# Kernel optimization log

Measured on AMD Instinct MI355X. Metric: run time of the kernel, lower is better.

The kernel has to match this reference:

```python
import jax, jax.numpy as jnp
import numpy as np

ALPHA = 200.0      # cfg.TRAIN.VOTING_ALPHA
RHO = 100.0        # ADMM penalty
SIGMA = 1e-3       # ADMM regularization
ITERS = 150        # fixed ADMM iterations


def _admm_qp(Q, q, C, l, u):
    n = Q.shape[0]
    K = Q + SIGMA * jnp.eye(n, dtype=Q.dtype) + RHO * (C.T @ C)
    cf = jax.scipy.linalg.cho_factor(K)
    x0 = jnp.zeros((n,), Q.dtype)
    z0 = jnp.clip(jnp.zeros((C.shape[0],), Q.dtype), l, u)
    y0 = jnp.zeros((C.shape[0],), Q.dtype)

    def step(carry, _):
        x, z, y = carry
        rhs = SIGMA * x - q + C.T @ (RHO * z - y)
        x = jax.scipy.linalg.cho_solve(cf, rhs)
        Cx = C @ x
        z = jnp.clip(Cx + y / RHO, l, u)
        y = y + RHO * (Cx - z)
        return (x, z, y), None

    (x, _, _), _ = jax.lax.scan(step, (x0, z0, y0), None, length=ITERS)
    return x


def _l2n(x, axis):
    return x / jnp.maximum(jnp.linalg.norm(x, axis=axis, keepdims=True), 1e-12)


def _forward(feat_tra, feat_det, iou_mat, W, b):
    n1, d = feat_tra.shape
    n2 = feat_det.shape[0]
    # cross-graph feature update
    Mp0 = feat_tra @ feat_det.T + iou_mat                      # (n1,n2)
    m1 = Mp0 @ feat_det                                        # (n1,d)
    m2 = Mp0.T @ feat_tra                                      # (n2,d)
    lam1 = jax.lax.stop_gradient(jnp.linalg.norm(feat_tra, axis=1, keepdims=True)
                                 / jnp.linalg.norm(m1, axis=1, keepdims=True))
    lam2 = jax.lax.stop_gradient(jnp.linalg.norm(feat_det, axis=1, keepdims=True)
                                 / jnp.linalg.norm(m2, axis=1, keepdims=True))
    e1 = jax.nn.relu((feat_tra + lam1 * m1) @ W.T + b)
    e2 = jax.nn.relu((feat_det + lam2 * m2) @ W.T + b)
    e1 = _l2n(e1, 1)
    e2 = _l2n(e2, 1)
    Mp = e1 @ e2.T                                             # (n1,n2) unary affinity
    P = Mp.T                                                   # (n2,n1)
    # Quadratic affinity: the torch code builds src_tgt[i,j,k,l] = <cat(e1_i,e1_j), cat(e2_k,e2_l)>
    # = Mp[i,k] + Mp[j,l], then gathers M[(a,c),(b,d)] = src_tgt[c,d,a,b]/2 masked by (a!=b)&(c!=d).
    ms = 1.0 - jnp.eye(n1, dtype=Mp.dtype)
    mt = 1.0 - jnp.eye(n2, dtype=Mp.dtype)
    M4 = 0.5 * (P[:, :, None, None] + P[None, None, :, :]) \
         * (mt[:, None, :, None] * ms[None, :, None, :])       # (n2,n1,n2,n1)
    n = n1 * n2
    Q = float((n1 - 1) * (n2 - 1)) * jnp.eye(n, dtype=Mp.dtype) - M4.reshape(n, n)
    q = -P.reshape(-1)                                         # -Mpp
    # equality constraints (square case): column sums and row sums == 1
    A = jnp.concatenate([jnp.kron(jnp.ones((1, n1)), jnp.eye(n2)),
                         jnp.kron(jnp.eye(n1), jnp.ones((1, n2)))], axis=0).astype(Mp.dtype)
    C = jnp.concatenate([jnp.eye(n, dtype=Mp.dtype), A], axis=0)
    l = jnp.concatenate([jnp.zeros((n,), Mp.dtype), jnp.ones((n1 + n2,), Mp.dtype)])
    u = jnp.concatenate([jnp.full((n,), 1e6, Mp.dtype), jnp.ones((n1 + n2,), Mp.dtype)])
    x = _admm_qp(Q, q, C, l, u)
    s = x.reshape(n2, n1).T                                    # (n1,n2)
    s = jnp.clip(s, 0.0, 1.0)                                  # relu(s) - relu(s-1)
    s = jax.nn.softmax(ALPHA * s, axis=-1)                     # Voting layer
    return s[None]                                             # (1,n1,n2)


def setup_inputs() -> dict:
    key = jax.random.key(0)
    k1, k2, k3, k4 = jax.random.split(key, 4)
    n1 = n2 = 64
    d = 512
    feat_tra = jax.random.normal(k1, (n1, d), jnp.float32)
    feat_det = jax.random.normal(k2, (n2, d), jnp.float32)
    iou_mat = jax.random.uniform(k3, (n1, n2), jnp.float32)
    W = jnp.eye(d, dtype=jnp.float32) + 0.01 * jax.random.normal(k4, (d, d), jnp.float32)
    b = jnp.zeros((d,), jnp.float32)
    return {"feat_tra": feat_tra, "feat_det": feat_det, "iou_mat": iou_mat, "W": W, "b": b}


def reference(feat_tra, feat_det, iou_mat, W, b):
    return _forward(feat_tra, feat_det, iou_mat, W, b)
```

## Files before the change

kernel.cpp:

```cpp
#include <hip/hip_runtime.h>
#include <math.h>

#define DD 512
#define NS 258
#define NSP 264
#define NWG 64
#define BLK 1024
#define RHO_ 100.0
#define SIG_ 1e-3
#define NITER 150
#define DELTA0 (3969.0 + SIG_ + RHO_)

typedef float v2f __attribute__((ext_vector_type(2)));

#define OFF_E1     512u
#define OFF_SUMS   512u
#define OFF_INV    4608u
#define OFF_E2     262656u
#define OFF_P      524800u
#define OFF_W      557568u
#define OFF_P32    590336u
#define OFF_W32    606720u
#define OFF_KSA    623104u
#define OFF_KSB    1168000u
#define OFF_N32    1712896u

__device__ __forceinline__ int perm258(int i){
  return (i < 128) ? i : (i == 128) ? 256 : (i == 129) ? 257 : (i - 2);
}

template<int CTRL>
__device__ __forceinline__ float dppadd(float v){
  int t = __builtin_amdgcn_mov_dpp(__float_as_int(v), CTRL, 0xF, 0xF, 1);
  return v + __int_as_float(t);
}
template<int CTRL>
__device__ __forceinline__ float dppmax(float v){
  int t = __builtin_amdgcn_mov_dpp(__float_as_int(v), CTRL, 0xF, 0xF, 1);
  return fmaxf(v, __int_as_float(t));
}
__device__ __forceinline__ float sum16(float v){
  v = dppadd<0xB1>(v);
  v = dppadd<0x4E>(v);
  v = dppadd<0x124>(v);
  v = dppadd<0x128>(v);
  return v;
}
__device__ __forceinline__ float wsum64f(float v){
  v = sum16(v);
  v += __shfl_xor(v, 16, 64);
  v += __shfl_xor(v, 32, 64);
  return v;
}
__device__ __forceinline__ float wmax64f(float v){
  v = dppmax<0xB1>(v); v = dppmax<0x4E>(v); v = dppmax<0x124>(v); v = dppmax<0x128>(v);
  v = fmaxf(v, __shfl_xor(v, 16, 64));
  v = fmaxf(v, __shfl_xor(v, 32, 64));
  return v;
}

__device__ __forceinline__ double gsum16d(double v){
  v += __shfl_xor(v, 1, 64);
  v += __shfl_xor(v, 2, 64);
  v += __shfl_xor(v, 4, 64);
  v += __shfl_xor(v, 8, 64);
  return v;
}
__device__ __forceinline__ double wsum64d(double v){
  v = gsum16d(v);
  v += __shfl_xor(v, 16, 64);
  v += __shfl_xor(v, 32, 64);
  return v;
}

__device__ __forceinline__ void decode_idx(int t, int& cls, int& pr, int& ix){
  if (t < 64)       { cls = 1; pr = 1; ix = t; }
  else if (t < 128) { cls = 2; pr = 1; ix = t - 64; }
  else if (t == 128){ cls = 0; pr = 1; ix = 0; }
  else if (t == 129){ cls = 0; pr = 0; ix = 0; }
  else if (t < 194) { cls = 1; pr = 0; ix = t - 130; }
  else              { cls = 2; pr = 0; ix = t - 194; }
}

__device__ __forceinline__ double ksval(int r, int c, const double* __restrict__ p,
                                        const double* __restrict__ w, const double* sumsL){
  int cr, prr, ir, cc, prc, ic;
  decode_idx(r, cr, prr, ir);
  decode_idx(c, cc, prc, ic);
  int m = prr + prc;
  double tval;
  if (cr == 0 && cc == 0)      tval = sumsL[m];
  else if (cr == 0 && cc == 1) tval = sumsL[8 + m*64 + ic];
  else if (cr == 1 && cc == 0) tval = sumsL[8 + m*64 + ir];
  else if (cr == 0 && cc == 2) tval = sumsL[200 + m*64 + ic];
  else if (cr == 2 && cc == 0) tval = sumsL[200 + m*64 + ir];
  else if (cr == 1 && cc == 1) tval = (ir == ic) ? sumsL[8 + m*64 + ir] : 0.0;
  else if (cr == 2 && cc == 2) tval = (ir == ic) ? sumsL[200 + m*64 + ir] : 0.0;
  else if (cr == 1 && cc == 2){
    double wv = w[ic*64 + ir], pv = p[ic*64 + ir];
    tval = (m == 0) ? wv : (m == 1) ? wv*pv : wv*pv*pv;
  } else {
    double wv = w[ir*64 + ic], pv = p[ir*64 + ic];
    tval = (m == 0) ? wv : (m == 1) ? wv*pv : wv*pv*pv;
  }
  double mv2 = 0.0;
  if (cr == 0 && cc == 0 && prr != prc) mv2 = -2.0;
  if (cr != 0 && cr == cc && ir == ic){
    if (prr != prc) mv2 = 2.0;
    else if (prr == 1) mv2 = -4.0 * RHO_;
  }
  return tval + mv2;
}

__global__ __launch_bounds__(BLK) void kp_feat(const float* __restrict__ ft,
                                               const float* __restrict__ fd,
                                               const float* __restrict__ iou,
                                               const float* __restrict__ Wm,
                                               const float* __restrict__ bb,
                                               char* ws){
  double* e1 = (double*)(ws + OFF_E1);
  double* e2 = (double*)(ws + OFF_E2);
  __shared__ double SH[1192];
  const int tid  = threadIdx.x;
  const int wg   = blockIdx.x;
  const int lane = tid & 63;
  const int wv   = tid >> 6;
  float* ftR = (float*)SH;
  float* fdR = ftR + 512;
  float* u1R = fdR + 512;
  float* u2R = u1R + 512;
  double* m0r = SH + 1024;
  double* m0c = m0r + 64;
  double* wp  = m0c + 64;
  double* sca = wp + 32;
  const int i = wg;
  if (tid < 512){ ftR[tid] = ft[i*DD + tid]; fdR[tid] = fd[i*DD + tid]; }
  {
    double nf = 0.0, nd = 0.0;
    if (tid < 512){
      float a = ftR[tid], b = fdR[tid];
      nf = (double)a*a; nd = (double)b*b;
    }
    nf = wsum64d(nf); nd = wsum64d(nd);
    if (lane == 0){ wp[wv] = nf; wp[16 + wv] = nd; }
    __syncthreads();
    if (tid == 0){
      double s0 = 0, s1 = 0;
      for (int q = 0; q < 16; ++q){ s0 += wp[q]; s1 += wp[16+q]; }
      sca[0] = s0; sca[1] = s1;
    }
  }
  {
    int j = tid >> 4, sub = tid & 15;
    double ar = 0.0, ac = 0.0;
    for (int t2 = 0; t2 < 32; ++t2){
      int k = t2*16 + sub;
      ar += (double)ftR[k] * (double)fd[(size_t)j*DD + k];
      ac += (double)fdR[k] * (double)ft[(size_t)j*DD + k];
    }
    ar = gsum16d(ar); ac = gsum16d(ac);
    if (sub == 0){
      m0r[j] = ar + (double)iou[i*64 + j];
      m0c[j] = ac + (double)iou[j*64 + i];
    }
  }
  __syncthreads();
  {
    int c = tid & 511, half = tid >> 9;
    const double* m0 = half ? m0c : m0r;
    const float*  FB = half ? ft  : fd;
    double a0 = 0, b0 = 0, c0 = 0, d0 = 0;
    for (int a2 = 0; a2 < 64; a2 += 4){
      a0 += m0[a2]   * (double)FB[(size_t)(a2  )*DD + c];
      b0 += m0[a2+1] * (double)FB[(size_t)(a2+1)*DD + c];
      c0 += m0[a2+2] * (double)FB[(size_t)(a2+2)*DD + c];
      d0 += m0[a2+3] * (double)FB[(size_t)(a2+3)*DD + c];
    }
    double mv = (a0 + b0) + (c0 + d0);
    double nn = wsum64d(mv*mv);
    if (lane == 0) wp[wv] = nn;
    __syncthreads();
    if (tid < 2){
      double s = 0;
      for (int q = tid*8; q < tid*8 + 8; ++q) s += wp[q];
      sca[2 + tid] = sqrt(sca[tid] / s);
    }
    __syncthreads();
    double l = sca[2 + half];
    float* uR = half ? u2R : u1R;
    const float* fR = half ? fdR : ftR;
    uR[c] = (float)((double)fR[c] + l*mv);
  }
  __syncthreads();
  {
    int c = tid & 511, half = tid >> 9;
    const float* uR  = half ? u2R : u1R;
    const float* wrp = Wm + (size_t)c*DD;
    double a0 = (double)bb[c], b0 = 0, c0 = 0, d0 = 0;
    for (int k = 0; k < DD; k += 4){
      float4 wq = *(const float4*)(wrp + k);
      float4 uq = *(const float4*)(uR + k);
      a0 += (double)uq.x*wq.x; b0 += (double)uq.y*wq.y;
      c0 += (double)uq.z*wq.z; d0 += (double)uq.w*wq.w;
    }
    double v = fmax((a0 + b0) + (c0 + d0), 0.0);
    double nn = wsum64d(v*v);
    if (lane == 0) wp[wv] = nn;
    __syncthreads();
    if (tid < 2){
      double s = 0;
      for (int q = tid*8; q < tid*8 + 8; ++q) s += wp[q];
      sca[4 + tid] = 1.0 / fmax(sqrt(s), 1e-12);
    }
    __syncthreads();
    double* e = half ? e2 : e1;
    e[(size_t)i*DD + c] = v * sca[4 + half];
  }
}

__global__ __launch_bounds__(BLK) void kp_pw(char* ws){
  const double* e1 = (const double*)(ws + OFF_E1);
  const double* e2 = (const double*)(ws + OFF_E2);
  double* p   = (double*)(ws + OFF_P);
  double* w   = (double*)(ws + OFF_W);
  float*  p32 = (float*) (ws + OFF_P32);
  float*  w32 = (float*) (ws + OFF_W32);
  __shared__ double e2R[512];
  const int tid = threadIdx.x;
  const int a = blockIdx.x;
  if (tid < 512) e2R[tid] = e2[(size_t)a*DD + tid];
  __syncthreads();
  int b = tid >> 4, sub = tid & 15;
  double a0 = 0.0, a1 = 0.0;
  for (int t2 = 0; t2 < 32; t2 += 2){
    a0 += e1[(size_t)b*DD + t2*16 + sub]     * e2R[t2*16 + sub];
    a1 += e1[(size_t)b*DD + (t2+1)*16 + sub] * e2R[(t2+1)*16 + sub];
  }
  double acc = gsum16d(a0 + a1);
  if (sub == 0){
    double pv = acc;
    double wv2 = 1.0 / (DELTA0 - pv);
    int jj = a*64 + b;
    p[jj] = pv; w[jj] = wv2; p32[jj] = (float)pv; w32[jj] = (float)wv2;
  }
}

__global__ __launch_bounds__(BLK) void kp_sums(char* ws){
  const double* p = (const double*)(ws + OFF_P);
  const double* w = (const double*)(ws + OFF_W);
  double* sumsG = (double*)(ws + OFF_SUMS);
  __shared__ double sumsL[456];
  const int tid = threadIdx.x;
  int a = tid >> 4, sub = tid & 15;
  {
    double r0 = 0, r1 = 0, r2 = 0;
    for (int b = sub*4; b < sub*4 + 4; ++b){
      double wv = w[a*64 + b], pv = p[a*64 + b];
      r0 += wv; r1 += wv*pv; r2 += wv*pv*pv;
    }
    r0 = gsum16d(r0); r1 = gsum16d(r1); r2 = gsum16d(r2);
    if (sub == 0){ sumsL[200 + a] = r0; sumsL[264 + a] = r1; sumsL[328 + a] = r2; }
  }
  {
    int b2 = tid >> 4;
    double c0 = 0, c1 = 0, c2 = 0;
    for (int a2 = sub*4; a2 < sub*4 + 4; ++a2){
      double wv = w[a2*64 + b2], pv = p[a2*64 + b2];
      c0 += wv; c1 += wv*pv; c2 += wv*pv*pv;
    }
    c0 = gsum16d(c0); c1 = gsum16d(c1); c2 = gsum16d(c2);
    if (sub == 0){ sumsL[8 + b2] = c0; sumsL[72 + b2] = c1; sumsL[136 + b2] = c2; }
  }
  __syncthreads();
  if (tid == 0){
    double t0 = 0, t1 = 0, t2 = 0;
    for (int a3 = 0; a3 < 64; ++a3){
      t0 += sumsL[200 + a3]; t1 += sumsL[264 + a3]; t2 += sumsL[328 + a3];
    }
    sumsL[0] = t0; sumsL[1] = t1; sumsL[2] = t2;
    sumsL[3] = 0; sumsL[4] = 0; sumsL[5] = 0; sumsL[6] = 0; sumsL[7] = 0;
  }
  if (tid >= 64 && tid < 128){
    int k = tid - 64;
    sumsL[392 + k] = 1.0 / (sumsL[136 + k] - 4.0*RHO_);
  }
  __syncthreads();
  for (int idx = tid; idx < 456; idx += BLK) sumsG[idx] = sumsL[idx];
}

template<int NC>
__device__ void p3_body(const double* __restrict__ p, const double* __restrict__ w,
                        const double* sumsL, const double* invd, double* temp,
                        double* __restrict__ KsB, int wg, int tid){
  if (tid < NC*64){
    int cidx = tid >> 6, k = tid & 63;
    int c = wg + 256*cidx;
    double tv;
    if (c < 64) tv = (k == c) ? invd[k] : 0.0;
    else        tv = ksval(k, c, p, w, sumsL) * invd[k];
    temp[cidx*68 + k] = tv;
  }
  __syncthreads();
  for (int idx = tid; idx < NS*NC; idx += BLK){
    int r = idx / NC, cidx = idx % NC;
    int c = wg + 256*cidx;
    double outv;
    if (r < 64){
      outv = temp[cidx*68 + r];
    } else {
      double first = (c < 64) ? 0.0 : ksval(r, c, p, w, sumsL);
      double acc = 0.0;
      const double* tp = temp + cidx*68;
      if (r < 128){
        const double* wr_ = w + (r-64)*64;
        const double* pr_ = p + (r-64)*64;
#pragma unroll 4
        for (int k = 0; k < 64; ++k){
          double pv = pr_[k];
          acc += wr_[k]*pv*pv*tp[k];
        }
      } else if (r == 128){
#pragma unroll 4
        for (int k = 0; k < 64; ++k) acc += sumsL[136 + k]*tp[k];
      } else if (r == 129){
#pragma unroll 4
        for (int k = 0; k < 64; ++k) acc += sumsL[72 + k]*tp[k];
      } else if (r < 194){
        int ir = r - 130;
        acc = (sumsL[72 + ir] + 2.0) * tp[ir];
      } else {
        int ir = r - 194;
        const double* wr_ = w + ir*64;
        const double* pr_ = p + ir*64;
#pragma unroll 4
        for (int k = 0; k < 64; ++k) acc += wr_[k]*pr_[k]*tp[k];
      }
      outv = first - acc;
    }
    KsB[(size_t)r*NSP + c] = outv;
  }
}

__global__ __launch_bounds__(BLK) void kp_p3(char* ws){
  const double* p = (const double*)(ws + OFF_P);
  const double* w = (const double*)(ws + OFF_W);
  const double* sumsG = (const double*)(ws + OFF_SUMS);
  double* KsB = (double*)(ws + OFF_KSB);
  __shared__ double sumsL[456];
  __shared__ double temp[136];
  const int tid = threadIdx.x, wg = blockIdx.x;
  for (int idx = tid; idx < 456; idx += BLK) sumsL[idx] = sumsG[idx];
  __syncthreads();
  if (wg < 2) p3_body<2>(p, w, sumsL, sumsL + 392, temp, KsB, wg, tid);
  else        p3_body<1>(p, w, sumsL, sumsL + 392, temp, KsB, wg, tid);
}

template<int MM>
__global__ __launch_bounds__(BLK) void kp_inv(const double* __restrict__ src, int p0,
                                              double* __restrict__ invG){
  __shared__ double Mbuf[2*4422];
  const int tid = threadIdx.x;
  double* cur = Mbuf;
  double* nxt = Mbuf + 4422;
  for (int idx = tid; idx < MM*MM; idx += BLK)
    cur[(idx/MM)*67 + (idx%MM)] = src[(size_t)(p0 + idx/MM)*NSP + p0 + idx%MM];
  __syncthreads();
  for (int k = 0; k < MM; ++k){
    double pk = 1.0 / cur[k*67 + k];
    for (int idx = tid; idx < MM*MM; idx += BLK){
      int i = idx/MM, j = idx%MM;
      double mkj = cur[k*67 + j];
      double nv;
      if (i == k){
        nv = (j == k) ? pk : mkj*pk;
      } else {
        double mik = cur[i*67 + k];
        nv = (j == k) ? (-mik*pk) : (cur[i*67 + j] - mik*(mkj*pk));
      }
      nxt[i*67 + j] = nv;
    }
    __syncthreads();
    double* t = cur; cur = nxt; nxt = t;
  }
  for (int idx = tid; idx < MM*MM; idx += BLK)
    invG[(idx/MM)*67 + idx%MM] = cur[(idx/MM)*67 + idx%MM];
}

template<int NC, int MM>
__device__ void apply_body(const double* __restrict__ src, double* __restrict__ dstD,
                           float* __restrict__ dstF, int p0, int wg, int tid,
                           const double* M, double* temp){
  for (int idx = tid; idx < NC*MM; idx += BLK){
    int cidx = idx / MM, k = idx % MM;
    int c = wg + 256*cidx;
    double tv;
    if (c >= p0 && c < p0 + MM){
      tv = M[k*67 + (c - p0)];
    } else {
      double a0 = 0.0, a1 = 0.0;
#pragma unroll 4
      for (int l = 0; l < MM; l += 2){
        a0 += M[k*67 + l]     * src[(size_t)(p0+l)*NSP + c];
        a1 += M[k*67 + l + 1] * src[(size_t)(p0+l+1)*NSP + c];
      }
      tv = a0 + a1;
    }
    temp[cidx*68 + k] = tv;
  }
  __syncthreads();
  for (int idx = tid; idx < NS*NC; idx += BLK){
    int r = idx / NC, cidx = idx % NC;
    int c = wg + 256*cidx;
    double val;
    if (r >= p0 && r < p0 + MM){
      val = temp[cidx*68 + (r - p0)];
    } else {
      double a0 = (c >= p0 && c < p0 + MM) ? 0.0 : src[(size_t)r*NSP + c];
      double a1 = 0.0;
#pragma unroll 4
      for (int k = 0; k < MM; k += 2){
        a0 -= src[(size_t)r*NSP + p0 + k]     * temp[cidx*68 + k];
        a1 += src[(size_t)r*NSP + p0 + k + 1] * temp[cidx*68 + k + 1];
      }
      val = a0 - a1;
    }
    if (dstD) dstD[(size_t)r*NSP + c] = val;
    else      dstF[perm258(r)*NSP + perm258(c)] = (float)val;
  }
}

template<int MM>
__global__ __launch_bounds__(BLK) void kp_apply(const double* __restrict__ src,
                                                double* __restrict__ dstD,
                                                float* __restrict__ dstF, int p0,
                                                const double* __restrict__ invG){
  __shared__ double M[4422];
  __shared__ double temp[136];
  const int tid = threadIdx.x, wg = blockIdx.x;
  for (int idx = tid; idx < MM*67; idx += BLK) M[idx] = invG[idx];
  __syncthreads();
  if (wg < 2) apply_body<2, MM>(src, dstD, dstF, p0, wg, tid, M, temp);
  else        apply_body<1, MM>(src, dstD, dstF, p0, wg, tid, M, temp);
}

__global__ __launch_bounds__(BLK) __attribute__((amdgpu_waves_per_eu(4, 4)))
void k_admm(const float* __restrict__ N32,
            const float* __restrict__ p32,
            const float* __restrict__ w32,
            float* __restrict__ out){
  __shared__ float2 tb[64][66];
  __shared__ float2 csTP[64][18];
  __shared__ float  csXl[64][18];
  __shared__ __align__(16) float s1f[264];
  __shared__ float s1g2[2];
  __shared__ float s2g[2];
  __shared__ __align__(16) float s2p[4][264];
  __shared__ float2 pairB[64];
  __shared__ float2 pairR[64];

  const int tid  = threadIdx.x;
  const int lane = tid & 63;
  const int wvid = tid >> 6;
  const int g    = tid >> 8;
  const int c    = tid & 255;

  float4 nc4[16];
#pragma unroll
  for (int k2 = 0; k2 < 16; ++k2){
    nc4[k2].x = N32[(64*g + 4*k2 + 0)*NSP + c];
    nc4[k2].y = N32[(64*g + 4*k2 + 1)*NSP + c];
    nc4[k2].z = N32[(64*g + 4*k2 + 2)*NSP + c];
    nc4[k2].w = N32[(64*g + 4*k2 + 3)*NSP + c];
  }
  const float ncg0 = N32[256*NSP + c];
  const float ncg1 = N32[257*NSP + c];

  float nr0 = 0.f, nr1 = 0.f, nr2 = 0.f, nr3 = 0.f, nrt0 = 0.f, nrt1 = 0.f;
  if (wvid == 4 || wvid == 5){
    int r = 252 + wvid;
    nr0 = N32[r*NSP + lane];       nr1 = N32[r*NSP + lane + 64];
    nr2 = N32[r*NSP + lane + 128]; nr3 = N32[r*NSP + lane + 192];
    nrt0 = N32[r*NSP + 256];       nrt1 = N32[r*NSP + 257];
  }

  float pr[4], wr[4], xr[4], vr[4], tq[4];
  double y2a[4], y2b = 0.0;
#pragma unroll
  for (int q = 0; q < 4; ++q){
    int j = (wvid*4 + q)*64 + lane;
    pr[q] = p32[j]; wr[q] = w32[j];
    xr[q] = 0.f; vr[q] = 0.f; tq[q] = 0.f; y2a[q] = 0.0;
  }
  __syncthreads();

  const int rid = tid >> 4, g16 = tid & 15;

  for (int it = 0; it < NITER; ++it){
    if (it){
      float ybs = 0.f;
#pragma unroll
      for (int s = 0; s < 8; ++s){
        float2 v2 = *(const float2*)&csXl[lane][2*s];
        ybs += v2.x + v2.y;
      }
      y2b += RHO_ * ((double)ybs - 1.0);
    }
    float base = (float)(2.0*RHO_ - y2b);
    float clt = 0.f, clp = 0.f;
#pragma unroll
    for (int q = 0; q < 4; ++q){
      float ya = (float)y2a[q];
      float rhs = 1e-3f*xr[q] + pr[q] + 100.f*fabsf(vr[q]) + base - ya;
      float t = wr[q]*rhs;
      float pt = pr[q]*t;
      tq[q] = t;
      tb[wvid*4 + q][lane] = make_float2(t, pt);
      clt += t; clp += pt;
    }
    csTP[lane][(wvid + lane) & 15] = make_float2(clt, clp);
    __syncthreads();

    {
      const float4 r0 = *(const float4*)&tb[rid][4*g16];
      const float4 r1 = *(const float4*)&tb[rid][4*g16 + 2];
      float st = (r0.x + r0.z) + (r1.x + r1.z);
      float sp = (r0.y + r0.w) + (r1.y + r1.w);
      st = sum16(st); sp = sum16(sp);
      if (g16 == (rid & 15)){ s1f[192 + rid] = st; s1f[64 + rid] = sp; }
      if (wvid == 0){
        float ct = 0.f, cp = 0.f;
#pragma unroll
        for (int s = 0; s < 8; ++s){
          float4 v4 = *(const float4*)&csTP[lane][2*s];
          ct += v4.x + v4.z; cp += v4.y + v4.w;
        }
        s1f[128 + lane] = ct; s1f[lane] = cp;
        float tt = wsum64f(ct);
        float tp = wsum64f(cp);
        if (lane == 0){ s1g2[1] = tt; s1g2[0] = tp; }
      }
    }
    __syncthreads();

    {
      float sv = s1f[64*g + lane];
      float a0 = 0.f, a1 = 0.f, a2 = 0.f, a3 = 0.f;
#pragma unroll
      for (int k2 = 0; k2 < 16; ++k2){
        float4 nq = nc4[k2];
        a0 += nq.x * __uint_as_float(__builtin_amdgcn_readlane(__float_as_uint(sv), 4*k2 + 0));
        a1 += nq.y * __uint_as_float(__builtin_amdgcn_readlane(__float_as_uint(sv), 4*k2 + 1));
        a2 += nq.z * __uint_as_float(__builtin_amdgcn_readlane(__float_as_uint(sv), 4*k2 + 2));
        a3 += nq.w * __uint_as_float(__builtin_amdgcn_readlane(__float_as_uint(sv), 4*k2 + 3));
      }
      float acc = (a0 + a1) + (a2 + a3);
      if (g == 0) acc += ncg0*s1g2[0] + ncg1*s1g2[1];
      s2p[g][c] = acc;
      if (wvid == 4 || wvid == 5){
        float a32 = nr0*s1f[lane] + nr1*s1f[lane+64]
                  + nr2*s1f[lane+128] + nr3*s1f[lane+192];
        a32 = wsum64f(a32);
        if (lane == 0) s2g[wvid - 4] = a32 + nrt0*s1g2[0] + nrt1*s1g2[1];
      }
    }
    __syncthreads();

    if (tid < 64){
      int b = tid;
      float sbE  = (s2p[0][128+b] + s2p[1][128+b]) + (s2p[2][128+b] + s2p[3][128+b]);
      float sbPE = (s2p[0][b] + s2p[1][b]) + (s2p[2][b] + s2p[3][b]);
      pairB[b] = make_float2(sbE, sbPE);
    } else if (tid < 128){
      int a = tid - 64;
      float sF  = (s2p[0][192+a] + s2p[1][192+a]) + (s2p[2][192+a] + s2p[3][192+a]);
      float sPF = (s2p[0][64+a] + s2p[1][64+a]) + (s2p[2][64+a] + s2p[3][64+a]);
      pairR[a] = make_float2(s2g[1] + sF, s2g[0] + sPF);
    }
    __syncthreads();

    {
      float2 pb = pairB[lane];
      float clx = 0.f;
#pragma unroll
      for (int q = 0; q < 4; ++q){
        int arow = wvid*4 + q;
        float2 prw = pairR[arow];
        float corr = prw.x + pb.x + pr[q]*(prw.y + pb.y);
        float xn = tq[q] - wr[q]*corr;
        vr[q] = xn + fminf(vr[q], 0.f);
        xr[q] = xn;
        float rsx = wsum64f(xn);
        y2a[q] += RHO_*((double)rsx - 1.0);
        clx += xn;
        if (it == NITER-1) ((float*)tb)[lane*68 + arow] = xn;
      }
      csXl[lane][(wvid + lane) & 15] = clx;
    }
    __syncthreads();
  }

  const float* xb = (const float*)tb;
#pragma unroll
  for (int q = 0; q < 4; ++q){
    int i = wvid*4 + q;
    float val = xb[i*68 + lane];
    val = fminf(fmaxf(val, 0.f), 1.f);
    float mx = wmax64f(val);
    float e = expf(200.f*(val - mx));
    float sm = wsum64f(e);
    out[i*64 + lane] = e / sm;
  }
}

extern "C" void kernel_launch(void* const* d_in, const int* in_sizes, int n_in,
                              void* d_out, int out_size, void* d_ws, size_t ws_size,
                              hipStream_t stream){
  (void)in_sizes; (void)n_in; (void)out_size; (void)ws_size;
  const float* ft  = (const float*)d_in[0];
  const float* fd  = (const float*)d_in[1];
  const float* iou = (const float*)d_in[2];
  const float* Wm  = (const float*)d_in[3];
  const float* bb  = (const float*)d_in[4];
  char* ws = (char*)d_ws;

  double* KsA  = (double*)(ws + OFF_KSA);
  double* KsB  = (double*)(ws + OFF_KSB);
  double* invG = (double*)(ws + OFF_INV);
  float*  N32  = (float*) (ws + OFF_N32);

  hipLaunchKernelGGL(kp_feat, dim3(NWG), dim3(BLK), 0, stream, ft, fd, iou, Wm, bb, ws);
  hipLaunchKernelGGL(kp_pw,   dim3(NWG), dim3(BLK), 0, stream, ws);
  hipLaunchKernelGGL(kp_sums, dim3(1),   dim3(BLK), 0, stream, ws);
  hipLaunchKernelGGL(kp_p3,   dim3(256), dim3(BLK), 0, stream, ws);

  hipLaunchKernelGGL(kp_inv<66>,   dim3(1),   dim3(BLK), 0, stream, KsB, 64, invG);
  hipLaunchKernelGGL(kp_apply<66>, dim3(256), dim3(BLK), 0, stream, KsB, KsA, (float*)nullptr, 64, invG);
  hipLaunchKernelGGL(kp_inv<64>,   dim3(1),   dim3(BLK), 0, stream, KsA, 130, invG);
  hipLaunchKernelGGL(kp_apply<64>, dim3(256), dim3(BLK), 0, stream, KsA, KsB, (float*)nullptr, 130, invG);
  hipLaunchKernelGGL(kp_inv<64>,   dim3(1),   dim3(BLK), 0, stream, KsB, 194, invG);
  hipLaunchKernelGGL(kp_apply<64>, dim3(256), dim3(BLK), 0, stream, KsB, (double*)nullptr, N32, 194, invG);

  const float* p32 = (const float*)(ws + OFF_P32);
  const float* w32 = (const float*)(ws + OFF_W32);
  hipLaunchKernelGGL(k_admm, dim3(1), dim3(BLK), 0, stream, N32, p32, w32, (float*)d_out);
}
```

Before: 807.7 us.

## Use one block per column with split-k reductions; atomics and DPP sums in ADMM loop

The p3 and apply kernels now launch one block per column (258 blocks) rather than 256 blocks with two columns on the first two. Each row's dot product is split over 4 lanes (8 for the apply temp vector) and combined with shuffles, so per-thread serial loops get shorter. In the ADMM loop, per-group partial sums go to a single shared array through shared-memory atomicAdd, removing one reduction pass and one barrier per iteration. Wave sums now use row-broadcast DPP plus readlane. The atomics change the float summation order and add LDS contention.

```diff
diff --git a/kernel.cpp b/kernel.cpp
--- a/kernel.cpp
+++ b/kernel.cpp
@@ -51,6 +51,12 @@
   v += __shfl_xor(v, 16, 64);
   v += __shfl_xor(v, 32, 64);
   return v;
+}
+__device__ __forceinline__ float wsum64u(float v){
+  v = sum16(v);
+  v = dppadd<0x142>(v);
+  v = dppadd<0x143>(v);
+  return __uint_as_float(__builtin_amdgcn_readlane(__float_as_uint(v), 63));
 }
 __device__ __forceinline__ float wmax64f(float v){
   v = dppmax<0xB1>(v); v = dppmax<0x4E>(v); v = dppmax<0x124>(v); v = dppmax<0x128>(v);
@@ -288,71 +294,56 @@
   for (int idx = tid; idx < 456; idx += BLK) sumsG[idx] = sumsL[idx];
 }
 
-template<int NC>
-__device__ void p3_body(const double* __restrict__ p, const double* __restrict__ w,
-                        const double* sumsL, const double* invd, double* temp,
-                        double* __restrict__ KsB, int wg, int tid){
-  if (tid < NC*64){
-    int cidx = tid >> 6, k = tid & 63;
-    int c = wg + 256*cidx;
-    double tv;
-    if (c < 64) tv = (k == c) ? invd[k] : 0.0;
-    else        tv = ksval(k, c, p, w, sumsL) * invd[k];
-    temp[cidx*68 + k] = tv;
-  }
-  __syncthreads();
-  for (int idx = tid; idx < NS*NC; idx += BLK){
-    int r = idx / NC, cidx = idx % NC;
-    int c = wg + 256*cidx;
-    double outv;
-    if (r < 64){
-      outv = temp[cidx*68 + r];
-    } else {
-      double first = (c < 64) ? 0.0 : ksval(r, c, p, w, sumsL);
-      double acc = 0.0;
-      const double* tp = temp + cidx*68;
-      if (r < 128){
-        const double* wr_ = w + (r-64)*64;
-        const double* pr_ = p + (r-64)*64;
-#pragma unroll 4
-        for (int k = 0; k < 64; ++k){
-          double pv = pr_[k];
-          acc += wr_[k]*pv*pv*tp[k];
-        }
-      } else if (r == 128){
-#pragma unroll 4
-        for (int k = 0; k < 64; ++k) acc += sumsL[136 + k]*tp[k];
-      } else if (r == 129){
-#pragma unroll 4
-        for (int k = 0; k < 64; ++k) acc += sumsL[72 + k]*tp[k];
-      } else if (r < 194){
-        int ir = r - 130;
-        acc = (sumsL[72 + ir] + 2.0) * tp[ir];
-      } else {
-        int ir = r - 194;
-        const double* wr_ = w + ir*64;
-        const double* pr_ = p + ir*64;
-#pragma unroll 4
-        for (int k = 0; k < 64; ++k) acc += wr_[k]*pr_[k]*tp[k];
-      }
-      outv = first - acc;
-    }
-    KsB[(size_t)r*NSP + c] = outv;
-  }
-}
-
 __global__ __launch_bounds__(BLK) void kp_p3(char* ws){
   const double* p = (const double*)(ws + OFF_P);
   const double* w = (const double*)(ws + OFF_W);
   const double* sumsG = (const double*)(ws + OFF_SUMS);
   double* KsB = (double*)(ws + OFF_KSB);
   __shared__ double sumsL[456];
-  __shared__ double temp[136];
-  const int tid = threadIdx.x, wg = blockIdx.x;
+  __shared__ double temp[68];
+  const int tid = threadIdx.x;
+  const int c = blockIdx.x;
   for (int idx = tid; idx < 456; idx += BLK) sumsL[idx] = sumsG[idx];
   __syncthreads();
-  if (wg < 2) p3_body<2>(p, w, sumsL, sumsL + 392, temp, KsB, wg, tid);
-  else        p3_body<1>(p, w, sumsL, sumsL + 392, temp, KsB, wg, tid);
+  const double* invd = sumsL + 392;
+  if (tid < 64){
+    int k = tid;
+    temp[k] = (c < 64) ? ((k == c) ? invd[k] : 0.0) : ksval(k, c, p, w, sumsL) * invd[k];
+  }
+  __syncthreads();
+  const double* tp = temp;
+  const int s = tid & 3;
+  auto dorow = [&](int rr){
+    if (rr < 64){
+      if (s == 0) KsB[(size_t)rr*NSP + c] = tp[rr];
+      return;
+    }
+    double acc = 0.0;
+    if (rr < 128){
+      const double* wr_ = w + (rr-64)*64;
+      const double* pr_ = p + (rr-64)*64;
+      for (int k = s; k < 64; k += 4){ double pv = pr_[k]; acc += wr_[k]*pv*pv*tp[k]; }
+    } else if (rr == 128){
+      for (int k = s; k < 64; k += 4) acc += sumsL[136 + k]*tp[k];
+    } else if (rr == 129){
+      for (int k = s; k < 64; k += 4) acc += sumsL[72 + k]*tp[k];
+    } else if (rr < 194){
+      if (s == 0){ int ir = rr - 130; acc = (sumsL[72 + ir] + 2.0)*tp[ir]; }
+    } else {
+      int ir = rr - 194;
+      const double* wr_ = w + ir*64;
+      const double* pr_ = p + ir*64;
+      for (int k = s; k < 64; k += 4) acc += wr_[k]*pr_[k]*tp[k];
+    }
+    acc += __shfl_xor(acc, 1, 64);
+    acc += __shfl_xor(acc, 2, 64);
+    if (s == 0){
+      double first = (c < 64) ? 0.0 : ksval(rr, c, p, w, sumsL);
+      KsB[(size_t)rr*NSP + c] = first - acc;
+    }
+  };
+  { int r = tid >> 2; if (r < 256) dorow(r); }
+  if (tid < 8) dorow(256 + (tid >> 2));
 }
 
 template<int MM>
@@ -386,61 +377,57 @@
     invG[(idx/MM)*67 + idx%MM] = cur[(idx/MM)*67 + idx%MM];
 }
 
-template<int NC, int MM>
-__device__ void apply_body(const double* __restrict__ src, double* __restrict__ dstD,
-                           float* __restrict__ dstF, int p0, int wg, int tid,
-                           const double* M, double* temp){
-  for (int idx = tid; idx < NC*MM; idx += BLK){
-    int cidx = idx / MM, k = idx % MM;
-    int c = wg + 256*cidx;
-    double tv;
-    if (c >= p0 && c < p0 + MM){
-      tv = M[k*67 + (c - p0)];
-    } else {
-      double a0 = 0.0, a1 = 0.0;
-#pragma unroll 4
-      for (int l = 0; l < MM; l += 2){
-        a0 += M[k*67 + l]     * src[(size_t)(p0+l)*NSP + c];
-        a1 += M[k*67 + l + 1] * src[(size_t)(p0+l+1)*NSP + c];
-      }
-      tv = a0 + a1;
-    }
-    temp[cidx*68 + k] = tv;
-  }
-  __syncthreads();
-  for (int idx = tid; idx < NS*NC; idx += BLK){
-    int r = idx / NC, cidx = idx % NC;
-    int c = wg + 256*cidx;
-    double val;
-    if (r >= p0 && r < p0 + MM){
-      val = temp[cidx*68 + (r - p0)];
-    } else {
-      double a0 = (c >= p0 && c < p0 + MM) ? 0.0 : src[(size_t)r*NSP + c];
-      double a1 = 0.0;
-#pragma unroll 4
-      for (int k = 0; k < MM; k += 2){
-        a0 -= src[(size_t)r*NSP + p0 + k]     * temp[cidx*68 + k];
-        a1 += src[(size_t)r*NSP + p0 + k + 1] * temp[cidx*68 + k + 1];
-      }
-      val = a0 - a1;
-    }
-    if (dstD) dstD[(size_t)r*NSP + c] = val;
-    else      dstF[perm258(r)*NSP + perm258(c)] = (float)val;
-  }
-}
-
 template<int MM>
 __global__ __launch_bounds__(BLK) void kp_apply(const double* __restrict__ src,
                                                 double* __restrict__ dstD,
                                                 float* __restrict__ dstF, int p0,
                                                 const double* __restrict__ invG){
   __shared__ double M[4422];
-  __shared__ double temp[136];
-  const int tid = threadIdx.x, wg = blockIdx.x;
+  __shared__ double temp[68];
+  __shared__ double srcMid[66];
+  const int tid = threadIdx.x;
+  const int c = blockIdx.x;
   for (int idx = tid; idx < MM*67; idx += BLK) M[idx] = invG[idx];
-  __syncthreads();
-  if (wg < 2) apply_body<2, MM>(src, dstD, dstF, p0, wg, tid, M, temp);
-  else        apply_body<1, MM>(src, dstD, dstF, p0, wg, tid, M, temp);
+  if (tid < MM) srcMid[tid] = src[(size_t)(p0 + tid)*NSP + c];
+  __syncthreads();
+  const bool cpiv = (c >= p0 && c < p0 + MM);
+  if (cpiv){
+    if (tid < MM) temp[tid] = M[tid*67 + (c - p0)];
+  } else {
+    int k = tid >> 3, s8 = tid & 7;
+    if (k < MM){
+      double a = 0.0;
+      for (int l = s8; l < MM; l += 8) a += M[k*67 + l]*srcMid[l];
+      a += __shfl_xor(a, 1, 64);
+      a += __shfl_xor(a, 2, 64);
+      a += __shfl_xor(a, 4, 64);
+      if (s8 == 0) temp[k] = a;
+    }
+  }
+  __syncthreads();
+  const int s = tid & 3;
+  auto dorow = [&](int rr){
+    if (rr >= p0 && rr < p0 + MM){
+      if (s == 0){
+        double val = temp[rr - p0];
+        if (dstD) dstD[(size_t)rr*NSP + c] = val;
+        else      dstF[perm258(rr)*NSP + perm258(c)] = (float)val;
+      }
+      return;
+    }
+    double acc = 0.0;
+    for (int k = s; k < MM; k += 4) acc += src[(size_t)rr*NSP + p0 + k]*temp[k];
+    acc += __shfl_xor(acc, 1, 64);
+    acc += __shfl_xor(acc, 2, 64);
+    if (s == 0){
+      double f = cpiv ? 0.0 : src[(size_t)rr*NSP + c];
+      double val = f - acc;
+      if (dstD) dstD[(size_t)rr*NSP + c] = val;
+      else      dstF[perm258(rr)*NSP + perm258(c)] = (float)val;
+    }
+  };
+  { int r = tid >> 2; if (r < 256) dorow(r); }
+  if (tid < 8) dorow(256 + (tid >> 2));
 }
 
 __global__ __launch_bounds__(BLK) __attribute__((amdgpu_waves_per_eu(4, 4)))
@@ -454,9 +441,7 @@
   __shared__ __align__(16) float s1f[264];
   __shared__ float s1g2[2];
   __shared__ float s2g[2];
-  __shared__ __align__(16) float s2p[4][264];
-  __shared__ float2 pairB[64];
-  __shared__ float2 pairR[64];
+  __shared__ float s2s[264];
 
   const int tid  = threadIdx.x;
   const int lane = tid & 63;
@@ -518,6 +503,7 @@
       clt += t; clp += pt;
     }
     csTP[lane][(wvid + lane) & 15] = make_float2(clt, clp);
+    if (tid < 264) s2s[tid] = 0.f;
     __syncthreads();
 
     {
@@ -535,8 +521,8 @@
           ct += v4.x + v4.z; cp += v4.y + v4.w;
         }
         s1f[128 + lane] = ct; s1f[lane] = cp;
-        float tt = wsum64f(ct);
-        float tp = wsum64f(cp);
+        float tt = wsum64u(ct);
+        float tp = wsum64u(cp);
         if (lane == 0){ s1g2[1] = tt; s1g2[0] = tp; }
       }
     }
@@ -555,41 +541,31 @@
       }
       float acc = (a0 + a1) + (a2 + a3);
       if (g == 0) acc += ncg0*s1g2[0] + ncg1*s1g2[1];
-      s2p[g][c] = acc;
+      atomicAdd(&s2s[c], acc);
       if (wvid == 4 || wvid == 5){
         float a32 = nr0*s1f[lane] + nr1*s1f[lane+64]
                   + nr2*s1f[lane+128] + nr3*s1f[lane+192];
-        a32 = wsum64f(a32);
+        a32 = wsum64u(a32);
         if (lane == 0) s2g[wvid - 4] = a32 + nrt0*s1g2[0] + nrt1*s1g2[1];
       }
     }
     __syncthreads();
 
-    if (tid < 64){
-      int b = tid;
-      float sbE  = (s2p[0][128+b] + s2p[1][128+b]) + (s2p[2][128+b] + s2p[3][128+b]);
-      float sbPE = (s2p[0][b] + s2p[1][b]) + (s2p[2][b] + s2p[3][b]);
-      pairB[b] = make_float2(sbE, sbPE);
-    } else if (tid < 128){
-      int a = tid - 64;
-      float sF  = (s2p[0][192+a] + s2p[1][192+a]) + (s2p[2][192+a] + s2p[3][192+a]);
-      float sPF = (s2p[0][64+a] + s2p[1][64+a]) + (s2p[2][64+a] + s2p[3][64+a]);
-      pairR[a] = make_float2(s2g[1] + sF, s2g[0] + sPF);
-    }
-    __syncthreads();
-
     {
-      float2 pb = pairB[lane];
+      float sbE  = s2s[128 + lane];
+      float sbPE = s2s[lane];
+      float g1 = s2g[1], g0 = s2g[0];
       float clx = 0.f;
 #pragma unroll
       for (int q = 0; q < 4; ++q){
         int arow = wvid*4 + q;
-        float2 prw = pairR[arow];
-        float corr = prw.x + pb.x + pr[q]*(prw.y + pb.y);
+        float sF  = s2s[192 + arow];
+        float sPF = s2s[64 + arow];
+        float corr = (g1 + sF) + sbE + pr[q]*((g0 + sPF) + sbPE);
         float xn = tq[q] - wr[q]*corr;
         vr[q] = xn + fminf(vr[q], 0.f);
         xr[q] = xn;
-        float rsx = wsum64f(xn);
+        float rsx = wsum64u(xn);
         y2a[q] += RHO_*((double)rsx - 1.0);
         clx += xn;
         if (it == NITER-1) ((float*)tb)[lane*68 + arow] = xn;
@@ -631,14 +607,14 @@
   hipLaunchKernelGGL(kp_feat, dim3(NWG), dim3(BLK), 0, stream, ft, fd, iou, Wm, bb, ws);
   hipLaunchKernelGGL(kp_pw,   dim3(NWG), dim3(BLK), 0, stream, ws);
   hipLaunchKernelGGL(kp_sums, dim3(1),   dim3(BLK), 0, stream, ws);
-  hipLaunchKernelGGL(kp_p3,   dim3(256), dim3(BLK), 0, stream, ws);
-
-  hipLaunchKernelGGL(kp_inv<66>,   dim3(1),   dim3(BLK), 0, stream, KsB, 64, invG);
-  hipLaunchKernelGGL(kp_apply<66>, dim3(256), dim3(BLK), 0, stream, KsB, KsA, (float*)nullptr, 64, invG);
-  hipLaunchKernelGGL(kp_inv<64>,   dim3(1),   dim3(BLK), 0, stream, KsA, 130, invG);
-  hipLaunchKernelGGL(kp_apply<64>, dim3(256), dim3(BLK), 0, stream, KsA, KsB, (float*)nullptr, 130, invG);
-  hipLaunchKernelGGL(kp_inv<64>,   dim3(1),   dim3(BLK), 0, stream, KsB, 194, invG);
-  hipLaunchKernelGGL(kp_apply<64>, dim3(256), dim3(BLK), 0, stream, KsB, (double*)nullptr, N32, 194, invG);
+  hipLaunchKernelGGL(kp_p3,   dim3(NS),  dim3(BLK), 0, stream, ws);
+
+  hipLaunchKernelGGL(kp_inv<66>,   dim3(1),  dim3(BLK), 0, stream, KsB, 64, invG);
+  hipLaunchKernelGGL(kp_apply<66>, dim3(NS), dim3(BLK), 0, stream, KsB, KsA, (float*)nullptr, 64, invG);
+  hipLaunchKernelGGL(kp_inv<64>,   dim3(1),  dim3(BLK), 0, stream, KsA, 130, invG);
+  hipLaunchKernelGGL(kp_apply<64>, dim3(NS), dim3(BLK), 0, stream, KsA, KsB, (float*)nullptr, 130, invG);
+  hipLaunchKernelGGL(kp_inv<64>,   dim3(1),  dim3(BLK), 0, stream, KsB, 194, invG);
+  hipLaunchKernelGGL(kp_apply<64>, dim3(NS), dim3(BLK), 0, stream, KsB, (double*)nullptr, N32, 194, invG);
 
   const float* p32 = (const float*)(ws + OFF_P32);
   const float* w32 = (const float*)(ws + OFF_W32);
```

Result: slower. 885.2 us (+9.6%).
